# Performance work log

Hardware: AMD Instinct MI355X
Metric: run time of the kernel (lower is better)

The kernel has to match this reference:

```python
import jax, jax.numpy as jnp
import numpy as np

N, E, F, U, H = 10000, 160000, 128, 128, 8
BN_EPS = 1e-3  # keras BatchNormalization default


def _batch_norm(x, gamma, beta):
    # GraphBatchNormalization in training mode: stats over the flat node/edge axis
    mean = jnp.mean(x, axis=0, keepdims=True)
    var = jnp.var(x, axis=0, keepdims=True)
    return (x - mean) * jax.lax.rsqrt(var + BN_EPS) * gamma + beta


def setup_inputs() -> dict:
    key = jax.random.key(0)
    k = jax.random.split(key, 12)
    s = 0.1  # weight init scale
    return {
        "node_attributes": jax.random.normal(k[0], (N, F), jnp.float32),
        "edge_attributes": jax.random.normal(k[1], (E, F), jnp.float32),
        "edge_indices": jax.random.randint(k[2], (E, 2), 0, N, jnp.int32),
        "W_edge": jax.random.normal(k[3], (3 * F, U), jnp.float32) * s,
        "b_edge": jnp.zeros((U,), jnp.float32),
        "gamma_e": jnp.ones((U,), jnp.float32),
        "beta_e": jnp.zeros((U,), jnp.float32),
        "W_node": jax.random.normal(k[4], (F, U), jnp.float32) * s,
        "b_node": jnp.zeros((U,), jnp.float32),
        "gamma_n": jnp.ones((U,), jnp.float32),
        "beta_n": jnp.zeros((U,), jnp.float32),
        "W_att": jax.random.normal(k[5], (H, F, U), jnp.float32) * s,
        "b_att": jnp.zeros((H, U), jnp.float32),
        "a_att": jax.random.normal(k[6], (H, 3 * U), jnp.float32) * s,
        "gru_kernel": jax.random.normal(k[7], (U, 3 * U), jnp.float32) * s,
        "gru_rkernel": jax.random.normal(k[8], (U, 3 * U), jnp.float32) * s,
        "gru_bias": jnp.zeros((2, 3 * U), jnp.float32),
    }


def reference(node_attributes, edge_attributes, edge_indices, W_edge, b_edge,
              gamma_e, beta_e, W_node, b_node, gamma_n, beta_n,
              W_att, b_att, a_att, gru_kernel, gru_rkernel, gru_bias):
    dst = edge_indices[:, 0]  # receiving (ingoing) node per edge
    src = edge_indices[:, 1]  # sending (outgoing) node per edge

    # gather -> concat -> edge MLP -> graph batch norm
    edge_in = node_attributes[src]   # GatherNodesOutgoing
    edge_out = node_attributes[dst]  # GatherNodesIngoing
    edge_concat = jnp.concatenate([edge_in, edge_out, edge_attributes], axis=-1)  # [E, 3F]
    edge_updated = jax.nn.relu(edge_concat @ W_edge + b_edge)
    edge_updated = _batch_norm(edge_updated, gamma_e, beta_e)  # [E, U]

    # multi-head GAT attention over edges, aggregated to receiving node
    z = jnp.einsum('nf,hfu->hnu', node_attributes, W_att) + b_att[:, None, :]  # [H,N,U]
    a_src, a_dst, a_edge = jnp.split(a_att, 3, axis=-1)  # each [H,U]
    s_src = jnp.einsum('hnu,hu->hn', z, a_src)[:, src]           # [H,E]
    s_dst = jnp.einsum('hnu,hu->hn', z, a_dst)[:, dst]           # [H,E]
    s_edge = jnp.einsum('eu,hu->he', edge_updated, a_edge)       # [H,E]
    logits = jax.nn.leaky_relu(s_src + s_dst + s_edge, 0.2)

    seg_max = jax.vmap(lambda l: jax.ops.segment_max(l, dst, num_segments=N))(logits)  # [H,N]
    ex = jnp.exp(logits - seg_max[:, dst])
    den = jax.vmap(lambda e: jax.ops.segment_sum(e, dst, num_segments=N))(ex)          # [H,N]
    alpha = ex / den[:, dst]                                                            # [H,E]

    msgs = alpha[:, :, None] * z[:, src]  # [H,E,U]
    agg = jax.vmap(lambda m: jax.ops.segment_sum(m, dst, num_segments=N))(msgs)  # [H,N,U]
    node_attended = jax.nn.relu(jnp.mean(agg, axis=0))  # [N,U]

    # node MLP + graph batch norm
    node_updated = jax.nn.relu(node_attributes @ W_node + b_node)
    node_updated = _batch_norm(node_updated, gamma_n, beta_n)  # [N,U]

    # GRU update (keras GRUCell, reset_after=True): input=node_attended, state=node_updated
    mx = node_attended @ gru_kernel + gru_bias[0]
    mi = node_updated @ gru_rkernel + gru_bias[1]
    xz, xr, xh = jnp.split(mx, 3, axis=-1)
    rz, rr, rh = jnp.split(mi, 3, axis=-1)
    zg = jax.nn.sigmoid(xz + rz)
    rg = jax.nn.sigmoid(xr + rr)
    hh = jnp.tanh(xh + rg * rh)
    node_final = zg * node_updated + (1.0 - zg) * hh

    return node_final, edge_updated
```

## Files before the change

kernel.cpp:

```cpp
#include <hip/hip_runtime.h>
#include <hip/hip_bf16.h>

#define NN 10000
#define EE 160000
#define FF 128
#define UU 128
#define HH 8
#define BN_EPS 1e-3f

typedef __attribute__((ext_vector_type(8))) short bf16x8;
typedef __attribute__((ext_vector_type(8))) unsigned short u16x8;
typedef __attribute__((ext_vector_type(4))) unsigned short u16x4;
typedef __attribute__((ext_vector_type(4))) unsigned int u32x4;
typedef __attribute__((ext_vector_type(4))) float f32x4;
typedef __attribute__((ext_vector_type(2))) float f32x2;

static __device__ __forceinline__ unsigned short f2bf(float f) {
    unsigned u = __float_as_uint(f);
    u += 0x7fffu + ((u >> 16) & 1u);
    return (unsigned short)(u >> 16);
}
static __device__ __forceinline__ float bf2f(unsigned short b) {
    return __uint_as_float((unsigned)b << 16);
}

__global__ void k_prep(const float* __restrict__ node, unsigned short* __restrict__ node_bf,
                       const float* __restrict__ We, unsigned short* __restrict__ WtE,
                       const float* __restrict__ Wn, unsigned short* __restrict__ WnT,
                       const float* __restrict__ Watt, unsigned short* __restrict__ WtA,
                       const float* __restrict__ Wk, const float* __restrict__ Wr,
                       unsigned short* __restrict__ WcT) {
    int b = blockIdx.x, t = threadIdx.x;
    if (b < 1250) {
        int i = b * 256 + t;
        float4 v = reinterpret_cast<const float4*>(node)[i];
        ushort4 o;
        o.x = f2bf(v.x); o.y = f2bf(v.y); o.z = f2bf(v.z); o.w = f2bf(v.w);
        reinterpret_cast<ushort4*>(node_bf)[i] = o;
    } else if (b < 1442) {
        int i = (b - 1250) * 256 + t;
        int s = i >> 14, rem = i & 16383, u = rem >> 7, k = rem & 127;
        WtE[i] = f2bf(We[(s * 128 + k) * 128 + u]);
    } else if (b < 1506) {
        int i = (b - 1442) * 256 + t;
        int k = i >> 7, u = i & 127;
        WnT[u * 128 + k] = f2bf(Wn[i]);
    } else if (b < 2018) {
        int i = (b - 1506) * 256 + t;
        int h = i >> 14, rem = i & 16383, f = rem >> 7, u = rem & 127;
        WtA[h * 16384 + u * 128 + f] = f2bf(Watt[i]);
    } else {
        int i = (b - 2018) * 256 + t;
        int c = i >> 8, k = i & 255;
        float v;
        if (c < 256)       v = (k < 128) ? Wk[k * 384 + c] : Wr[(k - 128) * 384 + c];
        else if (c < 384)  v = (k < 128) ? Wk[k * 384 + c] : 0.f;
        else               v = (k < 128) ? 0.f : Wr[(k - 128) * 384 + (c - 128)];
        WcT[c * 256 + k] = f2bf(v);
    }
}

__global__ void k_hist(const int* __restrict__ eidx, int* __restrict__ cnt, int E) {
    int e = blockIdx.x * 256 + threadIdx.x;
    if (e < E) atomicAdd(&cnt[eidx[2 * e]], 1);
}

__global__ void k_scan(const int* __restrict__ cnt, int* __restrict__ off,
                       int* __restrict__ cursor, int N) {
    __shared__ int wpre[16];
    __shared__ int runsh;
    int t = threadIdx.x, lane = t & 63, wv = t >> 6;
    if (t == 0) { off[0] = 0; runsh = 0; }
    __syncthreads();
    for (int base = 0; base < N; base += 1024) {
        int x = (base + t < N) ? cnt[base + t] : 0;
        int s = x;
#pragma unroll
        for (int o = 1; o < 64; o <<= 1) {
            int v = __shfl_up(s, o, 64);
            if (lane >= o) s += v;
        }
        if (lane == 63) wpre[wv] = s;
        __syncthreads();
        if (t == 0) {
            int acc = runsh;
#pragma unroll
            for (int i = 0; i < 16; ++i) { int tmp = wpre[i]; wpre[i] = acc; acc += tmp; }
            runsh = acc;
        }
        __syncthreads();
        int inc = s + wpre[wv];
        if (base + t < N) {
            off[base + t + 1] = inc;
            cursor[base + t] = inc - x;
        }
        __syncthreads();
    }
}

__global__ void k_scatter(const int* __restrict__ eidx, int* __restrict__ cursor,
                          int* __restrict__ elist, int* __restrict__ pos, int E) {
    int e = blockIdx.x * 256 + threadIdx.x;
    if (e < E) {
        int d = eidx[2 * e];
        int p = atomicAdd(&cursor[d], 1);
        elist[p] = e;
        pos[e] = p;
    }
}

__global__ void __launch_bounds__(256) k_z8(
        const unsigned short* __restrict__ node_bf, const unsigned short* __restrict__ WtA,
        const float* __restrict__ batt, const float* __restrict__ aatt,
        unsigned char* __restrict__ zt8, float* __restrict__ s_src, float* __restrict__ s_dst) {
    __shared__ unsigned short lds[16 * 1032];
    int n0 = blockIdx.x * 16;
    int t = threadIdx.x;
    {
        int r = t >> 4, c = t & 15;
        *reinterpret_cast<uint4*>(&lds[r * 136 + c * 8]) =
            *reinterpret_cast<const uint4*>(node_bf + (size_t)(n0 + r) * 128 + c * 8);
    }
    __syncthreads();

    int wid = t >> 6, lane = t & 63;
    int lr = lane & 15, lg = lane >> 4;

    f32x4 acc[2][8];
#pragma unroll
    for (int hh = 0; hh < 2; ++hh)
#pragma unroll
        for (int nt = 0; nt < 8; ++nt) acc[hh][nt] = (f32x4){0.f, 0.f, 0.f, 0.f};

#pragma unroll
    for (int ks = 0; ks < 4; ++ks) {
        int kb = ks * 32 + lg * 8;
        bf16x8 a = *reinterpret_cast<const bf16x8*>(&lds[lr * 136 + kb]);
#pragma unroll
        for (int hh = 0; hh < 2; ++hh) {
            const unsigned short* Wh = WtA + (size_t)(wid * 2 + hh) * 16384;
#pragma unroll
            for (int nt = 0; nt < 8; ++nt) {
                bf16x8 b = *reinterpret_cast<const bf16x8*>(Wh + (size_t)(nt * 16 + lr) * 128 + kb);
                acc[hh][nt] = __builtin_amdgcn_mfma_f32_16x16x32_bf16(a, b, acc[hh][nt], 0, 0, 0);
            }
        }
    }

    __syncthreads();
    int head0 = wid * 2, head1 = wid * 2 + 1;
    float ps[2][4], pd[2][4];
#pragma unroll
    for (int hh = 0; hh < 2; ++hh)
#pragma unroll
        for (int r = 0; r < 4; ++r) { ps[hh][r] = 0.f; pd[hh][r] = 0.f; }

#pragma unroll
    for (int nt = 0; nt < 8; ++nt) {
        int col = nt * 16 + lr;
        float b0 = batt[head0 * 128 + col], b1 = batt[head1 * 128 + col];
        float as0 = aatt[head0 * 384 + col], ad0 = aatt[head0 * 384 + 128 + col];
        float as1 = aatt[head1 * 384 + col], ad1 = aatt[head1 * 384 + 128 + col];
#pragma unroll
        for (int r = 0; r < 4; ++r) {
            int row = lg * 4 + r;
            float z0 = acc[0][nt][r] + b0;
            float z1 = acc[1][nt][r] + b1;
            unsigned pk = __builtin_amdgcn_cvt_pk_fp8_f32(z0, z1, 0, false);
            lds[row * 520 + col * 4 + wid] = (unsigned short)(pk & 0xffffu);
            ps[0][r] = fmaf(z0, as0, ps[0][r]);
            pd[0][r] = fmaf(z0, ad0, pd[0][r]);
            ps[1][r] = fmaf(z1, as1, ps[1][r]);
            pd[1][r] = fmaf(z1, ad1, pd[1][r]);
        }
    }
#pragma unroll
    for (int o = 1; o < 16; o <<= 1) {
#pragma unroll
        for (int hh = 0; hh < 2; ++hh)
#pragma unroll
            for (int r = 0; r < 4; ++r) {
                ps[hh][r] += __shfl_xor(ps[hh][r], o, 64);
                pd[hh][r] += __shfl_xor(pd[hh][r], o, 64);
            }
    }
    if (lr == 0) {
#pragma unroll
        for (int hh = 0; hh < 2; ++hh) {
            int head = wid * 2 + hh;
#pragma unroll
            for (int r = 0; r < 4; ++r) {
                int n = n0 + lg * 4 + r;
                s_src[n * 8 + head] = ps[hh][r];
                s_dst[n * 8 + head] = pd[hh][r];
            }
        }
    }
    __syncthreads();
    unsigned short* zt8u = reinterpret_cast<unsigned short*>(zt8);
    for (int q = t; q < 16 * 64; q += 256) {
        int row = q >> 6, c = q & 63;
        *reinterpret_cast<uint4*>(&zt8u[(size_t)(n0 + row) * 512 + c * 8]) =
            *reinterpret_cast<const uint4*>(&lds[row * 520 + c * 8]);
    }
}

__global__ void __launch_bounds__(256) k_p12_mfma(
        const unsigned short* __restrict__ node_bf, const unsigned short* __restrict__ WtE,
        unsigned short* __restrict__ p12, int N) {
    __shared__ unsigned short ash[64][136];
    int n0 = blockIdx.x * 64;
    int s = blockIdx.y;
    int t = threadIdx.x;
    for (int q = t; q < 64 * 16; q += 256) {
        int r = q >> 4, c = q & 15;
        int n = n0 + r; if (n >= N) n = N - 1;
        *reinterpret_cast<uint4*>(&ash[r][c * 8]) =
            *reinterpret_cast<const uint4*>(node_bf + (size_t)n * 128 + c * 8);
    }
    __syncthreads();

    int wid = t >> 6, lane = t & 63;
    int wm = wid >> 1, wn = wid & 1;
    int lr = lane & 15, lg = lane >> 4;

    f32x4 acc[2][4];
#pragma unroll
    for (int m = 0; m < 2; ++m)
#pragma unroll
        for (int n = 0; n < 4; ++n) acc[m][n] = (f32x4){0.f, 0.f, 0.f, 0.f};

    const unsigned short* Wh = WtE + (size_t)s * 16384;
#pragma unroll
    for (int ks = 0; ks < 4; ++ks) {
        int kb = ks * 32 + lg * 8;
        bf16x8 a0 = *reinterpret_cast<const bf16x8*>(&ash[wm * 32 + lr][kb]);
        bf16x8 a1 = *reinterpret_cast<const bf16x8*>(&ash[wm * 32 + 16 + lr][kb]);
        bf16x8 b[4];
#pragma unroll
        for (int n = 0; n < 4; ++n)
            b[n] = *reinterpret_cast<const bf16x8*>(Wh + (size_t)(wn * 64 + n * 16 + lr) * 128 + kb);
#pragma unroll
        for (int n = 0; n < 4; ++n) {
            acc[0][n] = __builtin_amdgcn_mfma_f32_16x16x32_bf16(a0, b[n], acc[0][n], 0, 0, 0);
            acc[1][n] = __builtin_amdgcn_mfma_f32_16x16x32_bf16(a1, b[n], acc[1][n], 0, 0, 0);
        }
    }

    __syncthreads();
    unsigned short* ot = &ash[0][0];
#pragma unroll
    for (int n = 0; n < 4; ++n) {
        int col = wn * 64 + n * 16 + lr;
#pragma unroll
        for (int m = 0; m < 2; ++m) {
            int rowb = wm * 32 + m * 16 + lg * 4;
#pragma unroll
            for (int r = 0; r < 4; ++r)
                ot[(rowb + r) * 136 + col] = f2bf(acc[m][n][r]);
        }
    }
    __syncthreads();
    for (int q = t; q < 64 * 16; q += 256) {
        int r = q >> 4, c = q & 15;
        int row = n0 + r;
        if (row < N)
            *reinterpret_cast<uint4*>(&p12[(size_t)row * 256 + s * 128 + c * 8]) =
                *reinterpret_cast<const uint4*>(&ot[r * 136 + c * 8]);
    }
}

__global__ void __launch_bounds__(256) k_pe_comb(
        const float* __restrict__ eattr, const unsigned short* __restrict__ WtE,
        const float* __restrict__ be, const unsigned short* __restrict__ p12,
        const int* __restrict__ eidx, unsigned short* __restrict__ ebuf,
        float* __restrict__ part) {
    __shared__ unsigned short ash[64][136];
    __shared__ unsigned short pcomb[64][136];
    __shared__ int sd[128];
    __shared__ float sbuf[4][64], qbuf[4][64];
    int e0 = blockIdx.x * 64;
    int t = threadIdx.x;
    if (t < 128) sd[t] = eidx[e0 * 2 + t];
    __syncthreads();
    for (int q = t; q < 64 * 32; q += 256) {
        int r = q >> 5, c = q & 31;
        f32x4 v = __builtin_nontemporal_load(
            reinterpret_cast<const f32x4*>(eattr + (size_t)(e0 + r) * 128 + c * 4));
        ushort4 o;
        o.x = f2bf(v.x); o.y = f2bf(v.y); o.z = f2bf(v.z); o.w = f2bf(v.w);
        *reinterpret_cast<ushort4*>(&ash[r][c * 4]) = o;
    }
    for (int q = t; q < 64 * 16; q += 256) {
        int r = q >> 4, c = q & 15;
        int dst = sd[r * 2], src = sd[r * 2 + 1];
        u16x8 a = *reinterpret_cast<const u16x8*>(p12 + (size_t)src * 256 + c * 8);
        u16x8 b = *reinterpret_cast<const u16x8*>(p12 + (size_t)dst * 256 + 128 + c * 8);
        u16x8 o;
#pragma unroll
        for (int j = 0; j < 8; ++j) o[j] = f2bf(bf2f(a[j]) + bf2f(b[j]));
        *reinterpret_cast<u16x8*>(&pcomb[r][c * 8]) = o;
    }
    __syncthreads();

    int wid = t >> 6, lane = t & 63;
    int wm = wid >> 1, wn = wid & 1;
    int lr = lane & 15, lg = lane >> 4;

    f32x4 acc[2][4];
#pragma unroll
    for (int m = 0; m < 2; ++m)
#pragma unroll
        for (int n = 0; n < 4; ++n) acc[m][n] = (f32x4){0.f, 0.f, 0.f, 0.f};

    const unsigned short* Wh = WtE + (size_t)2 * 16384;
#pragma unroll
    for (int ks = 0; ks < 4; ++ks) {
        int kb = ks * 32 + lg * 8;
        bf16x8 a0 = *reinterpret_cast<const bf16x8*>(&ash[wm * 32 + lr][kb]);
        bf16x8 a1 = *reinterpret_cast<const bf16x8*>(&ash[wm * 32 + 16 + lr][kb]);
        bf16x8 b[4];
#pragma unroll
        for (int n = 0; n < 4; ++n)
            b[n] = *reinterpret_cast<const bf16x8*>(Wh + (size_t)(wn * 64 + n * 16 + lr) * 128 + kb);
#pragma unroll
        for (int n = 0; n < 4; ++n) {
            acc[0][n] = __builtin_amdgcn_mfma_f32_16x16x32_bf16(a0, b[n], acc[0][n], 0, 0, 0);
            acc[1][n] = __builtin_amdgcn_mfma_f32_16x16x32_bf16(a1, b[n], acc[1][n], 0, 0, 0);
        }
    }

    __syncthreads();
    unsigned short* ot = &ash[0][0];
    float s[4] = {0.f, 0.f, 0.f, 0.f}, q[4] = {0.f, 0.f, 0.f, 0.f};
#pragma unroll
    for (int n = 0; n < 4; ++n) {
        int col = wn * 64 + n * 16 + lr;
        float bias = be[col];
#pragma unroll
        for (int m = 0; m < 2; ++m) {
            int rowb = wm * 32 + m * 16 + lg * 4;
#pragma unroll
            for (int r = 0; r < 4; ++r) {
                int row = rowb + r;
                float v = acc[m][n][r] + bias + bf2f(pcomb[row][col]);
                v = v > 0.f ? v : 0.f;
                ot[row * 136 + col] = f2bf(v);
                s[n] += v;
                q[n] += v * v;
            }
        }
    }
#pragma unroll
    for (int n = 0; n < 4; ++n) {
        s[n] += __shfl_xor(s[n], 16, 64);
        s[n] += __shfl_xor(s[n], 32, 64);
        q[n] += __shfl_xor(q[n], 16, 64);
        q[n] += __shfl_xor(q[n], 32, 64);
    }
    if (lane < 16) {
#pragma unroll
        for (int n = 0; n < 4; ++n) {
            sbuf[wid][n * 16 + lane] = s[n];
            qbuf[wid][n * 16 + lane] = q[n];
        }
    }
    __syncthreads();
    for (int q2 = t; q2 < 64 * 16; q2 += 256) {
        int r = q2 >> 4, c = q2 & 15;
        *reinterpret_cast<uint4*>(&ebuf[(size_t)(e0 + r) * 128 + c * 8]) =
            *reinterpret_cast<const uint4*>(&ot[r * 136 + c * 8]);
    }
    if (t < 128) {
        int half = t >> 6, c = t & 63;
        part[(size_t)blockIdx.x * 256 + t] = sbuf[half][c] + sbuf[2 + half][c];
        part[(size_t)blockIdx.x * 256 + 128 + t] = qbuf[half][c] + qbuf[2 + half][c];
    }
}

__global__ void __launch_bounds__(256) k_node_mlp_mfma(
        const unsigned short* __restrict__ node_bf, const unsigned short* __restrict__ WnT,
        const float* __restrict__ bn, unsigned short* __restrict__ nupd_bf,
        float* __restrict__ part, int N) {
    __shared__ unsigned short ash[64][136];
    __shared__ float sbuf[4][64], qbuf[4][64];
    int n0 = blockIdx.x * 64;
    int t = threadIdx.x;
    for (int q = t; q < 64 * 16; q += 256) {
        int r = q >> 4, c = q & 15;
        int n = n0 + r; if (n >= N) n = N - 1;
        *reinterpret_cast<uint4*>(&ash[r][c * 8]) =
            *reinterpret_cast<const uint4*>(node_bf + (size_t)n * 128 + c * 8);
    }
    __syncthreads();

    int wid = t >> 6, lane = t & 63;
    int wm = wid >> 1, wn = wid & 1;
    int lr = lane & 15, lg = lane >> 4;

    f32x4 acc[2][4];
#pragma unroll
    for (int m = 0; m < 2; ++m)
#pragma unroll
        for (int n = 0; n < 4; ++n) acc[m][n] = (f32x4){0.f, 0.f, 0.f, 0.f};

#pragma unroll
    for (int ks = 0; ks < 4; ++ks) {
        int kb = ks * 32 + lg * 8;
        bf16x8 a0 = *reinterpret_cast<const bf16x8*>(&ash[wm * 32 + lr][kb]);
        bf16x8 a1 = *reinterpret_cast<const bf16x8*>(&ash[wm * 32 + 16 + lr][kb]);
        bf16x8 b[4];
#pragma unroll
        for (int n = 0; n < 4; ++n)
            b[n] = *reinterpret_cast<const bf16x8*>(WnT + (size_t)(wn * 64 + n * 16 + lr) * 128 + kb);
#pragma unroll
        for (int n = 0; n < 4; ++n) {
            acc[0][n] = __builtin_amdgcn_mfma_f32_16x16x32_bf16(a0, b[n], acc[0][n], 0, 0, 0);
            acc[1][n] = __builtin_amdgcn_mfma_f32_16x16x32_bf16(a1, b[n], acc[1][n], 0, 0, 0);
        }
    }

    __syncthreads();
    unsigned short* ot = &ash[0][0];
    float s[4] = {0.f, 0.f, 0.f, 0.f}, q[4] = {0.f, 0.f, 0.f, 0.f};
#pragma unroll
    for (int n = 0; n < 4; ++n) {
        int col = wn * 64 + n * 16 + lr;
        float bias = bn[col];
#pragma unroll
        for (int m = 0; m < 2; ++m) {
            int rowb = wm * 32 + m * 16 + lg * 4;
#pragma unroll
            for (int r = 0; r < 4; ++r) {
                int row = n0 + rowb + r;
                float v = acc[m][n][r] + bias;
                v = v > 0.f ? v : 0.f;
                ot[(rowb + r) * 136 + col] = f2bf(v);
                if (row < N) { s[n] += v; q[n] += v * v; }
            }
        }
    }
#pragma unroll
    for (int n = 0; n < 4; ++n) {
        s[n] += __shfl_xor(s[n], 16, 64);
        s[n] += __shfl_xor(s[n], 32, 64);
        q[n] += __shfl_xor(q[n], 16, 64);
        q[n] += __shfl_xor(q[n], 32, 64);
    }
    if (lane < 16) {
#pragma unroll
        for (int n = 0; n < 4; ++n) {
            sbuf[wid][n * 16 + lane] = s[n];
            qbuf[wid][n * 16 + lane] = q[n];
        }
    }
    __syncthreads();
    for (int q2 = t; q2 < 64 * 16; q2 += 256) {
        int r = q2 >> 4, c = q2 & 15;
        int row = n0 + r;
        if (row < N)
            *reinterpret_cast<uint4*>(&nupd_bf[(size_t)row * 128 + c * 8]) =
                *reinterpret_cast<const uint4*>(&ot[r * 136 + c * 8]);
    }
    if (t < 128) {
        int half = t >> 6, c = t & 63;
        part[(size_t)blockIdx.x * 256 + t] = sbuf[half][c] + sbuf[2 + half][c];
        part[(size_t)blockIdx.x * 256 + 128 + t] = qbuf[half][c] + qbuf[2 + half][c];
    }
}

__global__ void k_bn_fin2(const float* __restrict__ part_e, int nblk_e, float invcnt_e,
                          const float* __restrict__ g_e, const float* __restrict__ b_e,
                          float* __restrict__ scale_e, float* __restrict__ shift_e,
                          const float* __restrict__ part_n, int nblk_n, float invcnt_n,
                          const float* __restrict__ g_n, const float* __restrict__ b_n,
                          float* __restrict__ scale_n, float* __restrict__ shift_n) {
    bool is_edge = blockIdx.x < 128;
    int u = is_edge ? blockIdx.x : blockIdx.x - 128;
    const float* part = is_edge ? part_e : part_n;
    int nblk = is_edge ? nblk_e : nblk_n;
    float invcnt = is_edge ? invcnt_e : invcnt_n;
    const float* g = is_edge ? g_e : g_n;
    const float* b = is_edge ? b_e : b_n;
    float* scale = is_edge ? scale_e : scale_n;
    float* shift = is_edge ? shift_e : shift_n;

    int t = threadIdx.x;
    float s = 0.f, q = 0.f;
    for (int i = t; i < nblk; i += 256) {
        s += part[(size_t)i * 256 + u];
        q += part[(size_t)i * 256 + 128 + u];
    }
    __shared__ float ls[4], lq[4];
    for (int o = 32; o > 0; o >>= 1) {
        s += __shfl_down(s, o, 64);
        q += __shfl_down(q, o, 64);
    }
    int lane = t & 63, w = t >> 6;
    if (lane == 0) { ls[w] = s; lq[w] = q; }
    __syncthreads();
    if (t == 0) {
        float S = ls[0] + ls[1] + ls[2] + ls[3];
        float Q = lq[0] + lq[1] + lq[2] + lq[3];
        float mean = S * invcnt;
        float var = Q * invcnt - mean * mean;
        float inv = rsqrtf(var + BN_EPS);
        float sc = g[u] * inv;
        scale[u] = sc;
        shift[u] = b[u] - mean * sc;
    }
}

__global__ void __launch_bounds__(256) k_edge_final(
        const unsigned short* __restrict__ ebuf, const float* __restrict__ scale,
        const float* __restrict__ shift, const float* __restrict__ aatt,
        const int* __restrict__ eidx, const int* __restrict__ pos,
        const float* __restrict__ s_src,
        float* __restrict__ eout, float* __restrict__ ls, int* __restrict__ srcl) {
    int t = threadIdx.x;
    int w = t >> 6, lane = t & 63;
    int q = lane & 31, half = lane >> 5;
    int e = blockIdx.x * 8 + w * 2 + half;

    float4 sc = *reinterpret_cast<const float4*>(scale + q * 4);
    float4 sh = *reinterpret_cast<const float4*>(shift + q * 4);
    float4 a4[8];
#pragma unroll
    for (int h = 0; h < 8; ++h)
        a4[h] = *reinterpret_cast<const float4*>(aatt + h * 384 + 256 + q * 4);

    ushort4 xb = *reinterpret_cast<const ushort4*>(ebuf + (size_t)e * 128 + q * 4);
    float4 x;
    x.x = bf2f(xb.x) * sc.x + sh.x;
    x.y = bf2f(xb.y) * sc.y + sh.y;
    x.z = bf2f(xb.z) * sc.z + sh.z;
    x.w = bf2f(xb.w) * sc.w + sh.w;
    *reinterpret_cast<float4*>(eout + (size_t)e * 128 + q * 4) = x;

    float v[8];
#pragma unroll
    for (int h = 0; h < 8; ++h)
        v[h] = x.x * a4[h].x + x.y * a4[h].y + x.z * a4[h].z + x.w * a4[h].w;
#pragma unroll
    for (int o = 1; o < 32; o <<= 1) {
#pragma unroll
        for (int h = 0; h < 8; ++h) v[h] += __shfl_xor(v[h], o, 64);
    }
    if (q == 0) {
        int src = eidx[2 * e + 1];
        int p = pos[e];
        srcl[p] = src;
        float4 a0 = *reinterpret_cast<const float4*>(s_src + (size_t)src * 8);
        float4 a1 = *reinterpret_cast<const float4*>(s_src + (size_t)src * 8 + 4);
        float4 o0, o1;
        o0.x = v[0] + a0.x; o0.y = v[1] + a0.y; o0.z = v[2] + a0.z; o0.w = v[3] + a0.w;
        o1.x = v[4] + a1.x; o1.y = v[5] + a1.y; o1.z = v[6] + a1.z; o1.w = v[7] + a1.w;
        *reinterpret_cast<float4*>(ls + (size_t)p * 8) = o0;
        *reinterpret_cast<float4*>(ls + (size_t)p * 8 + 4) = o1;
    }
}

__global__ void __launch_bounds__(256) k_agg(
        const unsigned char* __restrict__ zt8, const float* __restrict__ ls,
        const int* __restrict__ srcl, const float* __restrict__ s_dst,
        const int* __restrict__ off, unsigned short* __restrict__ cat) {
    int wv = threadIdx.x >> 6, lane = threadIdx.x & 63;
    int n = blockIdx.x * 4 + wv;
    __shared__ float wbuf[4][64][8];
    __shared__ int snbuf[4][64];

    int beg = off[n], end = off[n + 1];
    int deg = end - beg;
    if (deg == 0) {
        cat[(size_t)n * 256 + lane] = 0;
        cat[(size_t)n * 256 + 64 + lane] = 0;
        return;
    }

    float sdh[8];
#pragma unroll
    for (int h = 0; h < 8; ++h) sdh[h] = s_dst[n * 8 + h];

    float den[8], a0v[8], a1v[8];
#pragma unroll
    for (int h = 0; h < 8; ++h) { den[h] = 0.f; a0v[h] = 0.f; a1v[h] = 0.f; }

    for (int c0 = 0; c0 < deg; c0 += 64) {
        int cn = min(64, deg - c0);
        if (lane < cn) {
            int p = beg + c0 + lane;
            snbuf[wv][lane] = srcl[p];
            float4 l0 = *reinterpret_cast<const float4*>(ls + (size_t)p * 8);
            float4 l1 = *reinterpret_cast<const float4*>(ls + (size_t)p * 8 + 4);
            float lg[8] = {l0.x, l0.y, l0.z, l0.w, l1.x, l1.y, l1.z, l1.w};
#pragma unroll
            for (int h = 0; h < 8; ++h) {
                float x = lg[h] + sdh[h];
                x = x >= 0.f ? x : 0.2f * x;
                wbuf[wv][lane][h] = __expf(x);
            }
        }
        for (int i = 0; i < cn; ++i) {
            int sn_i = snbuf[wv][i];
            const unsigned char* zr = zt8 + (size_t)sn_i * 1024 + (size_t)lane * 8;
            uint2 zv0 = *reinterpret_cast<const uint2*>(zr);
            uint2 zv1 = *reinterpret_cast<const uint2*>(zr + 512);
            float4 w0 = *reinterpret_cast<const float4*>(&wbuf[wv][i][0]);
            float4 w1 = *reinterpret_cast<const float4*>(&wbuf[wv][i][4]);
            f32x2 q01 = __builtin_amdgcn_cvt_pk_f32_fp8(zv0.x, false);
            f32x2 q23 = __builtin_amdgcn_cvt_pk_f32_fp8(zv0.x, true);
            f32x2 q45 = __builtin_amdgcn_cvt_pk_f32_fp8(zv0.y, false);
            f32x2 q67 = __builtin_amdgcn_cvt_pk_f32_fp8(zv0.y, true);
            f32x2 r01 = __builtin_amdgcn_cvt_pk_f32_fp8(zv1.x, false);
            f32x2 r23 = __builtin_amdgcn_cvt_pk_f32_fp8(zv1.x, true);
            f32x2 r45 = __builtin_amdgcn_cvt_pk_f32_fp8(zv1.y, false);
            f32x2 r67 = __builtin_amdgcn_cvt_pk_f32_fp8(zv1.y, true);
            den[0] += w0.x; a0v[0] = fmaf(w0.x, q01.x, a0v[0]); a1v[0] = fmaf(w0.x, r01.x, a1v[0]);
            den[1] += w0.y; a0v[1] = fmaf(w0.y, q01.y, a0v[1]); a1v[1] = fmaf(w0.y, r01.y, a1v[1]);
            den[2] += w0.z; a0v[2] = fmaf(w0.z, q23.x, a0v[2]); a1v[2] = fmaf(w0.z, r23.x, a1v[2]);
            den[3] += w0.w; a0v[3] = fmaf(w0.w, q23.y, a0v[3]); a1v[3] = fmaf(w0.w, r23.y, a1v[3]);
            den[4] += w1.x; a0v[4] = fmaf(w1.x, q45.x, a0v[4]); a1v[4] = fmaf(w1.x, r45.x, a1v[4]);
            den[5] += w1.y; a0v[5] = fmaf(w1.y, q45.y, a0v[5]); a1v[5] = fmaf(w1.y, r45.y, a1v[5]);
            den[6] += w1.z; a0v[6] = fmaf(w1.z, q67.x, a0v[6]); a1v[6] = fmaf(w1.z, r67.x, a1v[6]);
            den[7] += w1.w; a0v[7] = fmaf(w1.w, q67.y, a0v[7]); a1v[7] = fmaf(w1.w, r67.y, a1v[7]);
        }
    }
    float r0 = 0.f, r1 = 0.f;
#pragma unroll
    for (int h = 0; h < 8; ++h) {
        float inv = 1.f / den[h];
        r0 = fmaf(a0v[h], inv, r0);
        r1 = fmaf(a1v[h], inv, r1);
    }
    cat[(size_t)n * 256 + lane] = f2bf(fmaxf(r0 * 0.125f, 0.f));
    cat[(size_t)n * 256 + 64 + lane] = f2bf(fmaxf(r1 * 0.125f, 0.f));
}

__global__ void k_gru_pre(const unsigned short* __restrict__ nupd_bf, const float* __restrict__ scale,
                          const float* __restrict__ shift, unsigned short* __restrict__ cat,
                          float* __restrict__ ush) {
    int i = blockIdx.x * 256 + threadIdx.x;
    if (i >= NN * 32) return;
    int n = i >> 5, j4 = (i & 31) * 4;
    ushort4 ub_in = *reinterpret_cast<const ushort4*>(nupd_bf + (size_t)n * 128 + j4);
    float4 sc = *reinterpret_cast<const float4*>(scale + j4);
    float4 sh = *reinterpret_cast<const float4*>(shift + j4);
    float4 uv;
    uv.x = bf2f(ub_in.x) * sc.x + sh.x;
    uv.y = bf2f(ub_in.y) * sc.y + sh.y;
    uv.z = bf2f(ub_in.z) * sc.z + sh.z;
    uv.w = bf2f(ub_in.w) * sc.w + sh.w;
    ushort4 ub;
    ub.x = f2bf(uv.x); ub.y = f2bf(uv.y); ub.z = f2bf(uv.z); ub.w = f2bf(uv.w);
    *reinterpret_cast<ushort4*>(cat + (size_t)n * 256 + 128 + j4) = ub;
    *reinterpret_cast<float4*>(ush + (size_t)n * 128 + j4) = uv;
}

__global__ void __launch_bounds__(256) k_gru_mm(
        const unsigned short* __restrict__ cat, const unsigned short* __restrict__ WcT,
        float* __restrict__ S, int N) {
    __shared__ unsigned short ash[64][264];
    int n0 = blockIdx.x * 64;
    int g = blockIdx.y;
    int t = threadIdx.x;
    for (int q = t; q < 64 * 32; q += 256) {
        int r = q >> 5, c = q & 31;
        int n = n0 + r; if (n >= N) n = N - 1;
        *reinterpret_cast<uint4*>(&ash[r][c * 8]) =
            *reinterpret_cast<const uint4*>(cat + (size_t)n * 256 + c * 8);
    }
    __syncthreads();

    int wid = t >> 6, lane = t & 63;
    int wm = wid >> 1, wn = wid & 1;
    int lr = lane & 15, lg = lane >> 4;

    f32x4 acc[2][4];
#pragma unroll
    for (int m = 0; m < 2; ++m)
#pragma unroll
        for (int n = 0; n < 4; ++n) acc[m][n] = (f32x4){0.f, 0.f, 0.f, 0.f};

    const unsigned short* Wg = WcT + (size_t)g * 128 * 256;
#pragma unroll
    for (int ks = 0; ks < 8; ++ks) {
        int kb = ks * 32 + lg * 8;
        bf16x8 a0 = *reinterpret_cast<const bf16x8*>(&ash[wm * 32 + lr][kb]);
        bf16x8 a1 = *reinterpret_cast<const bf16x8*>(&ash[wm * 32 + 16 + lr][kb]);
        bf16x8 b[4];
#pragma unroll
        for (int n = 0; n < 4; ++n)
            b[n] = *reinterpret_cast<const bf16x8*>(Wg + (size_t)(wn * 64 + n * 16 + lr) * 256 + kb);
#pragma unroll
        for (int n = 0; n < 4; ++n) {
            acc[0][n] = __builtin_amdgcn_mfma_f32_16x16x32_bf16(a0, b[n], acc[0][n], 0, 0, 0);
            acc[1][n] = __builtin_amdgcn_mfma_f32_16x16x32_bf16(a1, b[n], acc[1][n], 0, 0, 0);
        }
    }

    __syncthreads();
    float* otf = reinterpret_cast<float*>(&ash[0][0]);
#pragma unroll
    for (int n = 0; n < 4; ++n) {
        int col = wn * 64 + n * 16 + lr;
#pragma unroll
        for (int m = 0; m < 2; ++m) {
            int rowb = wm * 32 + m * 16 + lg * 4;
#pragma unroll
            for (int r = 0; r < 4; ++r)
                otf[(rowb + r) * 132 + col] = acc[m][n][r];
        }
    }
    __syncthreads();
    for (int q = t; q < 64 * 32; q += 256) {
        int r = q >> 5, c = q & 31;
        int row = n0 + r;
        if (row < N)
            *reinterpret_cast<float4*>(&S[(size_t)row * 512 + g * 128 + c * 4]) =
                *reinterpret_cast<const float4*>(&otf[r * 132 + c * 4]);
    }
}

__global__ void __launch_bounds__(256) k_gru_gates(
        const float* __restrict__ S, const float* __restrict__ ush,
        const float* __restrict__ gbias, float* __restrict__ outp) {
    int t = threadIdx.x;
    int n = blockIdx.x * 2 + (t >> 7);
    int u = t & 127;
    const float* b0 = gbias;
    const float* b1 = gbias + 384;
    float s0 = S[(size_t)n * 512 + u];
    float s1 = S[(size_t)n * 512 + 128 + u];
    float xh = S[(size_t)n * 512 + 256 + u];
    float rh = S[(size_t)n * 512 + 384 + u];
    float zg = 1.f / (1.f + __expf(-(s0 + b0[u] + b1[u])));
    float rg = 1.f / (1.f + __expf(-(s1 + b0[128 + u] + b1[128 + u])));
    float hh = tanhf(xh + b0[256 + u] + rg * (rh + b1[256 + u]));
    float uv = ush[(size_t)n * 128 + u];
    outp[(size_t)n * 128 + u] = zg * uv + (1.f - zg) * hh;
}

extern "C" void kernel_launch(void* const* d_in, const int* in_sizes, int n_in,
                              void* d_out, int out_size, void* d_ws, size_t ws_size,
                              hipStream_t stream) {
    const float* node    = (const float*)d_in[0];
    const float* eattr   = (const float*)d_in[1];
    const int*   eidx    = (const int*)d_in[2];
    const float* We      = (const float*)d_in[3];
    const float* be      = (const float*)d_in[4];
    const float* gamma_e = (const float*)d_in[5];
    const float* beta_e  = (const float*)d_in[6];
    const float* Wn      = (const float*)d_in[7];
    const float* bnb     = (const float*)d_in[8];
    const float* gamma_n = (const float*)d_in[9];
    const float* beta_n  = (const float*)d_in[10];
    const float* Watt    = (const float*)d_in[11];
    const float* batt    = (const float*)d_in[12];
    const float* aatt    = (const float*)d_in[13];
    const float* Wk      = (const float*)d_in[14];
    const float* Wr      = (const float*)d_in[15];
    const float* gbias   = (const float*)d_in[16];

    float* out_node = (float*)d_out;
    float* out_edge = out_node + (size_t)NN * UU;

    char* wp = (char*)d_ws;
    auto alloc = [&](size_t bytes) {
        void* p = (void*)wp;
        wp += (bytes + 255) / 256 * 256;
        return p;
    };
    unsigned char* zt8   = (unsigned char*)alloc((size_t)NN * 1024);
    unsigned short* ebuf = (unsigned short*)alloc((size_t)EE * 128 * 2);
    float* s_src   = (float*)alloc((size_t)NN * 8 * 4);
    float* s_dst   = (float*)alloc((size_t)NN * 8 * 4);
    float* lsbuf   = (float*)alloc((size_t)EE * 8 * 4);
    int*   srcl    = (int*)alloc((size_t)EE * 4);
    float* part_e  = (float*)alloc((size_t)2500 * 256 * 4);
    float* part_n  = (float*)alloc((size_t)157 * 256 * 4);
    float* scale_e = (float*)alloc(512);
    float* shift_e = (float*)alloc(512);
    float* scale_n = (float*)alloc(512);
    float* shift_n = (float*)alloc(512);
    unsigned short* nupd_bf = (unsigned short*)alloc((size_t)NN * 128 * 2);
    float* ush     = (float*)alloc((size_t)NN * 128 * 4);
    float* Sbuf    = (float*)alloc((size_t)NN * 512 * 4);
    int*   cnt     = (int*)alloc((size_t)NN * 4);
    int*   offs    = (int*)alloc((size_t)(NN + 1) * 4);
    int*   cursor  = (int*)alloc((size_t)NN * 4);
    int*   elist   = (int*)alloc((size_t)EE * 4);
    int*   pos     = (int*)alloc((size_t)EE * 4);
    unsigned short* node_bf = (unsigned short*)alloc((size_t)NN * 128 * 2);
    unsigned short* WtE     = (unsigned short*)alloc((size_t)3 * 128 * 128 * 2);
    unsigned short* WtA     = (unsigned short*)alloc((size_t)8 * 128 * 128 * 2);
    unsigned short* WnT     = (unsigned short*)alloc((size_t)128 * 128 * 2);
    unsigned short* WcT     = (unsigned short*)alloc((size_t)512 * 256 * 2);
    unsigned short* cat     = (unsigned short*)alloc((size_t)NN * 256 * 2);
    unsigned short* p12     = (unsigned short*)alloc((size_t)NN * 256 * 2);

    hipMemsetAsync(cnt, 0, (size_t)NN * 4, stream);
    k_hist<<<(EE + 255) / 256, 256, 0, stream>>>(eidx, cnt, EE);
    k_scan<<<1, 1024, 0, stream>>>(cnt, offs, cursor, NN);
    k_scatter<<<(EE + 255) / 256, 256, 0, stream>>>(eidx, cursor, elist, pos, EE);

    k_prep<<<2530, 256, 0, stream>>>(node, node_bf, We, WtE, Wn, WnT, Watt, WtA, Wk, Wr, WcT);

    k_z8<<<NN / 16, 256, 0, stream>>>(node_bf, WtA, batt, aatt, zt8, s_src, s_dst);
    k_node_mlp_mfma<<<(NN + 63) / 64, 256, 0, stream>>>(node_bf, WnT, bnb, nupd_bf, part_n, NN);

    k_p12_mfma<<<dim3((NN + 63) / 64, 2), 256, 0, stream>>>(node_bf, WtE, p12, NN);
    k_pe_comb<<<EE / 64, 256, 0, stream>>>(eattr, WtE, be, p12, eidx, ebuf, part_e);
    k_bn_fin2<<<256, 256, 0, stream>>>(part_e, EE / 64, 1.f / (float)EE, gamma_e, beta_e, scale_e, shift_e,
                                       part_n, (NN + 63) / 64, 1.f / (float)NN, gamma_n, beta_n, scale_n, shift_n);
    k_edge_final<<<EE / 8, 256, 0, stream>>>(ebuf, scale_e, shift_e, aatt, eidx, pos, s_src,
                                             out_edge, lsbuf, srcl);

    k_agg<<<NN / 4, 256, 0, stream>>>(zt8, lsbuf, srcl, s_dst, offs, cat);
    k_gru_pre<<<(NN * 32 + 255) / 256, 256, 0, stream>>>(nupd_bf, scale_n, shift_n, cat, ush);
    k_gru_mm<<<dim3((NN + 63) / 64, 4), 256, 0, stream>>>(cat, WcT, Sbuf, NN);
    k_gru_gates<<<NN / 2, 256, 0, stream>>>(Sbuf, ush, gbias, out_node);
}
```

Baseline: 240.1 us.

## Fuse GRU gate computation into the GRU matmul kernel epilogue

The GRU matmul now computes all four 128-column gate groups in one block, holding 32 accumulator vectors per lane, and applies sigmoid/tanh gating in the epilogue. This removes the [N,512] fp32 S buffer, the fp32 ush buffer and the separate gates kernel launch, cutting global memory traffic. The cost is a quarter as many blocks (157), higher register pressure that may lower occupancy, and a recomputed batch-norm state from bf16 instead of the fp32 copy.

```diff
diff --git a/kernel.cpp b/kernel.cpp
--- a/kernel.cpp
+++ b/kernel.cpp
@@ -637,31 +637,28 @@
 }
 
 __global__ void k_gru_pre(const unsigned short* __restrict__ nupd_bf, const float* __restrict__ scale,
-                          const float* __restrict__ shift, unsigned short* __restrict__ cat,
-                          float* __restrict__ ush) {
+                          const float* __restrict__ shift, unsigned short* __restrict__ cat) {
     int i = blockIdx.x * 256 + threadIdx.x;
     if (i >= NN * 32) return;
     int n = i >> 5, j4 = (i & 31) * 4;
     ushort4 ub_in = *reinterpret_cast<const ushort4*>(nupd_bf + (size_t)n * 128 + j4);
     float4 sc = *reinterpret_cast<const float4*>(scale + j4);
     float4 sh = *reinterpret_cast<const float4*>(shift + j4);
-    float4 uv;
-    uv.x = bf2f(ub_in.x) * sc.x + sh.x;
-    uv.y = bf2f(ub_in.y) * sc.y + sh.y;
-    uv.z = bf2f(ub_in.z) * sc.z + sh.z;
-    uv.w = bf2f(ub_in.w) * sc.w + sh.w;
     ushort4 ub;
-    ub.x = f2bf(uv.x); ub.y = f2bf(uv.y); ub.z = f2bf(uv.z); ub.w = f2bf(uv.w);
+    ub.x = f2bf(bf2f(ub_in.x) * sc.x + sh.x);
+    ub.y = f2bf(bf2f(ub_in.y) * sc.y + sh.y);
+    ub.z = f2bf(bf2f(ub_in.z) * sc.z + sh.z);
+    ub.w = f2bf(bf2f(ub_in.w) * sc.w + sh.w);
     *reinterpret_cast<ushort4*>(cat + (size_t)n * 256 + 128 + j4) = ub;
-    *reinterpret_cast<float4*>(ush + (size_t)n * 128 + j4) = uv;
-}
-
-__global__ void __launch_bounds__(256) k_gru_mm(
+}
+
+__global__ void __launch_bounds__(256) k_gru_fused(
         const unsigned short* __restrict__ cat, const unsigned short* __restrict__ WcT,
-        float* __restrict__ S, int N) {
+        const unsigned short* __restrict__ nupd_bf, const float* __restrict__ scale,
+        const float* __restrict__ shift, const float* __restrict__ gbias,
+        float* __restrict__ outp, int N) {
     __shared__ unsigned short ash[64][264];
     int n0 = blockIdx.x * 64;
-    int g = blockIdx.y;
     int t = threadIdx.x;
     for (int q = t; q < 64 * 32; q += 256) {
         int r = q >> 5, c = q & 31;
@@ -675,26 +672,28 @@
     int wm = wid >> 1, wn = wid & 1;
     int lr = lane & 15, lg = lane >> 4;
 
-    f32x4 acc[2][4];
-#pragma unroll
-    for (int m = 0; m < 2; ++m)
-#pragma unroll
-        for (int n = 0; n < 4; ++n) acc[m][n] = (f32x4){0.f, 0.f, 0.f, 0.f};
-
-    const unsigned short* Wg = WcT + (size_t)g * 128 * 256;
+    f32x4 acc[4][2][4];
+#pragma unroll
+    for (int g = 0; g < 4; ++g)
+#pragma unroll
+        for (int m = 0; m < 2; ++m)
+#pragma unroll
+            for (int n = 0; n < 4; ++n) acc[g][m][n] = (f32x4){0.f, 0.f, 0.f, 0.f};
+
 #pragma unroll
     for (int ks = 0; ks < 8; ++ks) {
         int kb = ks * 32 + lg * 8;
         bf16x8 a0 = *reinterpret_cast<const bf16x8*>(&ash[wm * 32 + lr][kb]);
         bf16x8 a1 = *reinterpret_cast<const bf16x8*>(&ash[wm * 32 + 16 + lr][kb]);
-        bf16x8 b[4];
-#pragma unroll
-        for (int n = 0; n < 4; ++n)
-            b[n] = *reinterpret_cast<const bf16x8*>(Wg + (size_t)(wn * 64 + n * 16 + lr) * 256 + kb);
-#pragma unroll
-        for (int n = 0; n < 4; ++n) {
-            acc[0][n] = __builtin_amdgcn_mfma_f32_16x16x32_bf16(a0, b[n], acc[0][n], 0, 0, 0);
-            acc[1][n] = __builtin_amdgcn_mfma_f32_16x16x32_bf16(a1, b[n], acc[1][n], 0, 0, 0);
+#pragma unroll
+        for (int g = 0; g < 4; ++g) {
+            const unsigned short* Wg = WcT + (size_t)g * 128 * 256;
+#pragma unroll
+            for (int n = 0; n < 4; ++n) {
+                bf16x8 b = *reinterpret_cast<const bf16x8*>(Wg + (size_t)(wn * 64 + n * 16 + lr) * 256 + kb);
+                acc[g][0][n] = __builtin_amdgcn_mfma_f32_16x16x32_bf16(a0, b, acc[g][0][n], 0, 0, 0);
+                acc[g][1][n] = __builtin_amdgcn_mfma_f32_16x16x32_bf16(a1, b, acc[g][1][n], 0, 0, 0);
+            }
         }
     }
 
@@ -703,12 +702,25 @@
 #pragma unroll
     for (int n = 0; n < 4; ++n) {
         int col = wn * 64 + n * 16 + lr;
+        float bz  = gbias[col] + gbias[384 + col];
+        float br  = gbias[128 + col] + gbias[384 + 128 + col];
+        float bxh = gbias[256 + col];
+        float brh = gbias[384 + 256 + col];
+        float sc = scale[col], sh = shift[col];
 #pragma unroll
         for (int m = 0; m < 2; ++m) {
             int rowb = wm * 32 + m * 16 + lg * 4;
 #pragma unroll
-            for (int r = 0; r < 4; ++r)
-                otf[(rowb + r) * 132 + col] = acc[m][n][r];
+            for (int r = 0; r < 4; ++r) {
+                int row = rowb + r;
+                int grow = n0 + row;
+                int gr = grow < N ? grow : N - 1;
+                float zg = 1.f / (1.f + __expf(-(acc[0][m][n][r] + bz)));
+                float rg = 1.f / (1.f + __expf(-(acc[1][m][n][r] + br)));
+                float hh = tanhf(acc[2][m][n][r] + bxh + rg * (acc[3][m][n][r] + brh));
+                float uv = bf2f(nupd_bf[(size_t)gr * 128 + col]) * sc + sh;
+                otf[row * 132 + col] = zg * uv + (1.f - zg) * hh;
+            }
         }
     }
     __syncthreads();
@@ -716,28 +728,9 @@
         int r = q >> 5, c = q & 31;
         int row = n0 + r;
         if (row < N)
-            *reinterpret_cast<float4*>(&S[(size_t)row * 512 + g * 128 + c * 4]) =
+            *reinterpret_cast<float4*>(&outp[(size_t)row * 128 + c * 4]) =
                 *reinterpret_cast<const float4*>(&otf[r * 132 + c * 4]);
     }
-}
-
-__global__ void __launch_bounds__(256) k_gru_gates(
-        const float* __restrict__ S, const float* __restrict__ ush,
-        const float* __restrict__ gbias, float* __restrict__ outp) {
-    int t = threadIdx.x;
-    int n = blockIdx.x * 2 + (t >> 7);
-    int u = t & 127;
-    const float* b0 = gbias;
-    const float* b1 = gbias + 384;
-    float s0 = S[(size_t)n * 512 + u];
-    float s1 = S[(size_t)n * 512 + 128 + u];
-    float xh = S[(size_t)n * 512 + 256 + u];
-    float rh = S[(size_t)n * 512 + 384 + u];
-    float zg = 1.f / (1.f + __expf(-(s0 + b0[u] + b1[u])));
-    float rg = 1.f / (1.f + __expf(-(s1 + b0[128 + u] + b1[128 + u])));
-    float hh = tanhf(xh + b0[256 + u] + rg * (rh + b1[256 + u]));
-    float uv = ush[(size_t)n * 128 + u];
-    outp[(size_t)n * 128 + u] = zg * uv + (1.f - zg) * hh;
 }
 
 extern "C" void kernel_launch(void* const* d_in, const int* in_sizes, int n_in,
@@ -783,8 +776,6 @@
     float* scale_n = (float*)alloc(512);
     float* shift_n = (float*)alloc(512);
     unsigned short* nupd_bf = (unsigned short*)alloc((size_t)NN * 128 * 2);
-    float* ush     = (float*)alloc((size_t)NN * 128 * 4);
-    float* Sbuf    = (float*)alloc((size_t)NN * 512 * 4);
     int*   cnt     = (int*)alloc((size_t)NN * 4);
     int*   offs    = (int*)alloc((size_t)(NN + 1) * 4);
     int*   cursor  = (int*)alloc((size_t)NN * 4);
@@ -816,7 +807,7 @@
                                              out_edge, lsbuf, srcl);
 
     k_agg<<<NN / 4, 256, 0, stream>>>(zt8, lsbuf, srcl, s_dst, offs, cat);
-    k_gru_pre<<<(NN * 32 + 255) / 256, 256, 0, stream>>>(nupd_bf, scale_n, shift_n, cat, ush);
-    k_gru_mm<<<dim3((NN + 63) / 64, 4), 256, 0, stream>>>(cat, WcT, Sbuf, NN);
-    k_gru_gates<<<NN / 2, 256, 0, stream>>>(Sbuf, ush, gbias, out_node);
-}
+    k_gru_pre<<<(NN * 32 + 255) / 256, 256, 0, stream>>>(nupd_bf, scale_n, shift_n, cat);
+    k_gru_fused<<<(NN + 63) / 64, 256, 0, stream>>>(cat, WcT, nupd_bf, scale_n, shift_n,
+                                                    gbias, out_node, NN);
+}
```

Result: slower. 256.7 us (+6.9%).
